# Performance work log

Hardware: AMD Instinct MI355X
Metric: run time of the kernel (lower is better)

## Reference

```python
import jax, jax.numpy as jnp
import numpy as np

N, B, T = 2048, 16, 256

def setup_inputs() -> dict:
    key = jax.random.key(0)
    k1, k2, k3, k4 = jax.random.split(key, 4)
    x = jax.random.normal(k1, (B, T, N), dtype=jnp.float32)
    weight = jax.random.normal(k2, (T, T), dtype=jnp.float32) * (1.0 / np.sqrt(T))
    bias = jax.random.normal(k3, (T,), dtype=jnp.float32) * 0.01
    # Gumbel(0,1) noise, matching torch.nn.functional.gumbel_softmax internals
    u = jax.random.uniform(k4, (N * N, 2), dtype=jnp.float32, minval=1e-6, maxval=1.0 - 1e-6)
    gumbel = -jnp.log(-jnp.log(u))
    return {"x": x, "weight": weight, "bias": bias, "gumbel": gumbel}

def reference(x, weight, bias, gumbel):
    # x: [B, T, N] -> node-major [N, B, T]
    xp = jnp.transpose(x, (2, 0, 1))
    n = xp.shape[0]
    # --- similarity-based logits (torch writes via .data -> no grad path) ---
    xs = jax.lax.stop_gradient(xp)
    x_avg = xs.mean(axis=1)                                          # [N, T]
    x_norm = x_avg / jnp.maximum(jnp.linalg.norm(x_avg, axis=-1, keepdims=True), 1e-12)
    sim = (x_norm @ x_norm.T + 1.0) * 0.5                            # [N, N] in [0,1]
    sim_flat = sim.reshape(-1)
    # gumbel_softmax(hard=True) forward: adjacency = argmax over (logits + g)
    score0 = sim_flat + gumbel[:, 0]
    score1 = (1.0 - sim_flat) + gumbel[:, 1]
    adj = (score0 > score1).astype(xp.dtype).reshape(n, n)           # directed adjacency
    # --- structural coefficient (dense, faithful to compute_structural_coeff) ---
    adj_sym = jnp.clip(adj + adj.T, 0.0, 1.0)
    nmask = jnp.clip(adj_sym + jnp.eye(n, dtype=xp.dtype), 0.0, 1.0)
    common = nmask @ nmask.T                                         # common-neighbor counts
    max_common = common.max()                                        # >= 1 (diagonal)
    valid = (adj_sym * (common > 1.0).astype(xp.dtype)) > 0
    struct = jnp.where(valid, (common / max_common) * common, 0.0)   # lambda_val = 1.0
    # edge weights only at directed-edge positions
    W = adj * struct                                                 # [src, dst]
    # --- gcn_norm (no self loops, improved=False): deg over dst, D^-1/2 W D^-1/2 ---
    deg = W.sum(axis=0)
    dinv = jnp.where(deg > 0, deg ** -0.5, 0.0)
    Wn = dinv[:, None] * W * dinv[None, :]
    # --- linear + gather-multiply-scatter aggregation (out[d] = sum_s Wn[s,d] x[s]) ---
    xw = jnp.einsum('nbt,to->nbo', xp, weight)                       # [N, B, T]
    out = jnp.einsum('sd,sbt->dbt', Wn, xw) + bias                   # [N, B, T]
    return jnp.transpose(out, (1, 2, 0))                             # [B, T, N]
```

## Files before the change

kernel.cpp:

```cpp
#include <hip/hip_runtime.h>

#define NN 2048
#define BB 16
#define TT 256

typedef unsigned short ushort_t;
typedef short bf16x8 __attribute__((ext_vector_type(8)));
typedef float f32x4 __attribute__((ext_vector_type(4)));

__device__ __forceinline__ ushort_t f2bf(float f) {
    unsigned u = __float_as_uint(f);
    return (ushort_t)((u + 0x7FFFu + ((u >> 16) & 1u)) >> 16);
}

__device__ __forceinline__ void gload16(const void* g, void* l) {
    __builtin_amdgcn_global_load_lds((const __attribute__((address_space(1))) unsigned int*)g,
                                     (__attribute__((address_space(3))) unsigned int*)l,
                                     16, 0, 0);
}

__device__ __forceinline__ void mfma_loop128(
    const ushort_t* __restrict__ Ag, size_t lda,
    const ushort_t* __restrict__ Bg, size_t ldb,
    int m0, int n0, int nkt,
    ushort_t (*As)[128][32], ushort_t (*Bs)[128][32],
    f32x4 (&acc)[4][4], int tid)
{
    const int lane = tid & 63, wave = tid >> 6;
    const int wr = wave >> 1, wc = wave & 1;
    const int r0 = tid >> 2, kc = (tid & 3) * 8;
    const int lr = lane & 15, kg = (lane >> 4) * 8;
    gload16(&Ag[(size_t)(m0 + r0) * lda + kc], &As[0][r0][kc]);
    gload16(&Bg[(size_t)(n0 + r0) * ldb + kc], &Bs[0][r0][kc]);
    gload16(&Ag[(size_t)(m0 + r0 + 64) * lda + kc], &As[0][r0 + 64][kc]);
    gload16(&Bg[(size_t)(n0 + r0 + 64) * ldb + kc], &Bs[0][r0 + 64][kc]);
    __syncthreads();
    int cur = 0;
    for (int kt = 0; kt < nkt; kt++) {
        if (kt + 1 < nkt) {
            const int k0 = (kt + 1) * 32;
            gload16(&Ag[(size_t)(m0 + r0) * lda + k0 + kc], &As[cur ^ 1][r0][kc]);
            gload16(&Bg[(size_t)(n0 + r0) * ldb + k0 + kc], &Bs[cur ^ 1][r0][kc]);
            gload16(&Ag[(size_t)(m0 + r0 + 64) * lda + k0 + kc], &As[cur ^ 1][r0 + 64][kc]);
            gload16(&Bg[(size_t)(n0 + r0 + 64) * ldb + k0 + kc], &Bs[cur ^ 1][r0 + 64][kc]);
        }
        bf16x8 af[4], bf[4];
#pragma unroll
        for (int f = 0; f < 4; f++) {
            af[f] = *(const bf16x8*)&As[cur][wr * 64 + f * 16 + lr][kg];
            bf[f] = *(const bf16x8*)&Bs[cur][wc * 64 + f * 16 + lr][kg];
        }
#pragma unroll
        for (int i = 0; i < 4; i++)
#pragma unroll
            for (int j = 0; j < 4; j++)
                acc[i][j] = __builtin_amdgcn_mfma_f32_16x16x32_bf16(af[i], bf[j], acc[i][j], 0, 0, 0);
        __syncthreads();
        cur ^= 1;
    }
}

__global__ __launch_bounds__(256) void k_colsum(const float* __restrict__ x,
                                                float* __restrict__ xsumT,
                                                float* __restrict__ ssq) {
    const int n = blockIdx.x * 256 + threadIdx.x;
    const int t = blockIdx.y;
    float s = 0.f;
#pragma unroll
    for (int b = 0; b < BB; b++) s += x[(size_t)(b * TT + t) * NN + n];
    xsumT[(size_t)t * NN + n] = s;
    atomicAdd(&ssq[n], s * s);
}

__global__ __launch_bounds__(256) void k_adj(const float* __restrict__ A,
                                             const float* __restrict__ ssq,
                                             const float* __restrict__ gumbel,
                                             ushort_t* __restrict__ adjb) {
    __shared__ __align__(16) float As[2][32][64];
    __shared__ __align__(16) float Bs[2][32][64];
    const int m0 = blockIdx.y * 64, n0 = blockIdx.x * 64;
    const int tid = threadIdx.x;
    const int tx = tid & 15, ty = tid >> 4;
    const int sr = tid >> 4, sc = (tid & 15) * 4;
    float acc[4][4];
#pragma unroll
    for (int i = 0; i < 4; i++)
#pragma unroll
        for (int j = 0; j < 4; j++) acc[i][j] = 0.f;
    gload16(&A[(size_t)sr * NN + m0 + sc], &As[0][sr][sc]);
    gload16(&A[(size_t)sr * NN + n0 + sc], &Bs[0][sr][sc]);
    gload16(&A[(size_t)(sr + 16) * NN + m0 + sc], &As[0][sr + 16][sc]);
    gload16(&A[(size_t)(sr + 16) * NN + n0 + sc], &Bs[0][sr + 16][sc]);
    __syncthreads();
    int cur = 0;
    for (int kt = 0; kt < 8; kt++) {
        if (kt + 1 < 8) {
            const int k0 = (kt + 1) * 32;
            gload16(&A[(size_t)(k0 + sr) * NN + m0 + sc], &As[cur ^ 1][sr][sc]);
            gload16(&A[(size_t)(k0 + sr) * NN + n0 + sc], &Bs[cur ^ 1][sr][sc]);
            gload16(&A[(size_t)(k0 + sr + 16) * NN + m0 + sc], &As[cur ^ 1][sr + 16][sc]);
            gload16(&A[(size_t)(k0 + sr + 16) * NN + n0 + sc], &Bs[cur ^ 1][sr + 16][sc]);
        }
#pragma unroll 16
        for (int kk = 0; kk < 32; kk++) {
            float4 a = *(const float4*)&As[cur][kk][ty * 4];
            float4 b = *(const float4*)&Bs[cur][kk][tx * 4];
            const float av[4] = {a.x, a.y, a.z, a.w};
            const float bv[4] = {b.x, b.y, b.z, b.w};
#pragma unroll
            for (int i = 0; i < 4; i++)
#pragma unroll
                for (int j = 0; j < 4; j++) acc[i][j] = fmaf(av[i], bv[j], acc[i][j]);
        }
        __syncthreads();
        cur ^= 1;
    }
    float invi[4], invj[4];
#pragma unroll
    for (int i = 0; i < 4; i++) {
        const float si = ssq[m0 + ty * 4 + i];
        invi[i] = (si > 0.f) ? rsqrtf(si) : 0.f;
        const float sj = ssq[n0 + tx * 4 + i];
        invj[i] = (sj > 0.f) ? rsqrtf(sj) : 0.f;
    }
#pragma unroll
    for (int i = 0; i < 4; i++) {
        const int gi = m0 + ty * 4 + i;
        const size_t rowb = (size_t)gi * NN + n0 + tx * 4;
#pragma unroll
        for (int j = 0; j < 4; j++) {
            const float dot = acc[i][j] * invi[i] * invj[j];
            const float2 g = *(const float2*)&gumbel[2 * (rowb + j)];
            adjb[rowb + j] = (dot > g.y - g.x) ? (ushort_t)0x3F80 : (ushort_t)0;
        }
    }
}

__global__ __launch_bounds__(256) void k_nmask(const ushort_t* __restrict__ adjb,
                                               ushort_t* __restrict__ nm) {
    __shared__ ushort_t tt[32][33];
    const int J = blockIdx.x * 32, I = blockIdx.y * 32;
    const int c = threadIdx.x & 31, r0 = threadIdx.x >> 5;
#pragma unroll
    for (int r = r0; r < 32; r += 8) tt[r][c] = adjb[(size_t)(J + r) * NN + I + c];
    __syncthreads();
#pragma unroll
    for (int r = r0; r < 32; r += 8) {
        const int gi = I + r, gj = J + c;
        const bool on = (gi == gj) || adjb[(size_t)gi * NN + gj] || tt[c][r];
        nm[(size_t)gi * NN + gj] = on ? (ushort_t)0x3F80 : (ushort_t)0;
    }
}

__global__ __launch_bounds__(256) void k_commonW(const ushort_t* __restrict__ nm,
                                                 const ushort_t* __restrict__ adjb,
                                                 float* __restrict__ W,
                                                 float* __restrict__ deg) {
    __shared__ __align__(16) ushort_t As[2][128][32];
    __shared__ __align__(16) ushort_t Bs[2][128][32];
    const int m0 = blockIdx.y * 128, n0 = blockIdx.x * 128;
    const int tid = threadIdx.x;
    const int lane = tid & 63, wave = tid >> 6;
    const int wr = wave >> 1, wc = wave & 1;
    f32x4 acc[4][4];
#pragma unroll
    for (int i = 0; i < 4; i++)
#pragma unroll
        for (int j = 0; j < 4; j++) acc[i][j] = (f32x4){0.f, 0.f, 0.f, 0.f};
    mfma_loop128(nm, NN, nm, NN, m0, n0, NN / 32, As, Bs, acc, tid);
    const int lr = lane & 15, rg = (lane >> 4) * 4;
#pragma unroll
    for (int j = 0; j < 4; j++) {
        const int gj = n0 + wc * 64 + j * 16 + lr;
        float psum = 0.f;
#pragma unroll
        for (int i = 0; i < 4; i++)
#pragma unroll
            for (int r = 0; r < 4; r++) {
                const int gi = m0 + wr * 64 + i * 16 + rg + r;
                const float cv = acc[i][j][r];
                const size_t fl = (size_t)gi * NN + gj;
                const float wv = (cv > 1.0f && adjb[fl]) ? cv * cv : 0.f;
                W[fl] = wv;
                psum += wv;
            }
        atomicAdd(&deg[gj], psum);
    }
}

__global__ __launch_bounds__(256) void k_wtn(const float* __restrict__ W,
                                             const float* __restrict__ deg,
                                             ushort_t* __restrict__ Wtn) {
    __shared__ float tt[64][65];
    const int S0 = blockIdx.x * 64, D0 = blockIdx.y * 64;
    const int c = threadIdx.x & 63, r0 = threadIdx.x >> 6;
#pragma unroll
    for (int r = r0; r < 64; r += 4) tt[r][c] = W[(size_t)(S0 + r) * NN + D0 + c];
    __syncthreads();
    const float dgs = deg[S0 + c];
    const float ds = (dgs > 0.f) ? rsqrtf(dgs) : 0.f;
#pragma unroll
    for (int r = r0; r < 64; r += 4) {
        const int d = D0 + r;
        const float dgd = deg[d];
        const float dd = (dgd > 0.f) ? rsqrtf(dgd) : 0.f;
        Wtn[(size_t)d * NN + S0 + c] = f2bf(tt[c][r] * ds * dd);
    }
}

__global__ __launch_bounds__(256) void k_xt(const float* __restrict__ x,
                                            ushort_t* __restrict__ xT) {
    __shared__ float tile[64][65];
    const int b = blockIdx.z, t0 = blockIdx.y * 64, n0 = blockIdx.x * 64;
    const int c = threadIdx.x & 63, r0 = threadIdx.x >> 6;
#pragma unroll
    for (int r = r0; r < 64; r += 4)
        tile[r][c] = x[(size_t)(b * TT + t0 + r) * NN + n0 + c];
    __syncthreads();
#pragma unroll
    for (int r = r0; r < 64; r += 4)
        xT[(size_t)(b * NN + n0 + r) * TT + t0 + c] = f2bf(tile[c][r]);
}

__global__ __launch_bounds__(256) void k_wt(const float* __restrict__ w,
                                            ushort_t* __restrict__ wT) {
    __shared__ float tile[64][65];
    const int t0 = blockIdx.y * 64, o0 = blockIdx.x * 64;
    const int c = threadIdx.x & 63, r0 = threadIdx.x >> 6;
#pragma unroll
    for (int r = r0; r < 64; r += 4)
        tile[r][c] = w[(size_t)(t0 + r) * TT + o0 + c];
    __syncthreads();
#pragma unroll
    for (int r = r0; r < 64; r += 4)
        wT[(size_t)(o0 + r) * TT + t0 + c] = f2bf(tile[c][r]);
}

__global__ __launch_bounds__(256) void k_xw(const ushort_t* __restrict__ wT,
                                            const ushort_t* __restrict__ xT,
                                            ushort_t* __restrict__ xwT) {
    __shared__ __align__(16) ushort_t As[2][128][32];
    __shared__ __align__(16) ushort_t Bs[2][128][32];
    const int b = blockIdx.z;
    const ushort_t* __restrict__ Bg = xT + (size_t)b * NN * TT;
    const int m0 = blockIdx.y * 128, n0 = blockIdx.x * 128;
    const int tid = threadIdx.x;
    const int lane = tid & 63, wave = tid >> 6;
    const int wr = wave >> 1, wc = wave & 1;
    f32x4 acc[4][4];
#pragma unroll
    for (int i = 0; i < 4; i++)
#pragma unroll
        for (int j = 0; j < 4; j++) acc[i][j] = (f32x4){0.f, 0.f, 0.f, 0.f};
    mfma_loop128(wT, TT, Bg, TT, m0, n0, TT / 32, As, Bs, acc, tid);
    const int lr = lane & 15, rg = (lane >> 4) * 4;
#pragma unroll
    for (int i = 0; i < 4; i++)
#pragma unroll
        for (int j = 0; j < 4; j++)
#pragma unroll
            for (int r = 0; r < 4; r++) {
                const int o = m0 + wr * 64 + i * 16 + rg + r;
                const int n = n0 + wc * 64 + j * 16 + lr;
                xwT[((size_t)b * TT + o) * NN + n] = f2bf(acc[i][j][r]);
            }
}

__global__ __launch_bounds__(256) void k_out(const ushort_t* __restrict__ xwT,
                                             const ushort_t* __restrict__ Wtn,
                                             const float* __restrict__ bias,
                                             float* __restrict__ out) {
    __shared__ __align__(16) ushort_t As[2][128][32];
    __shared__ __align__(16) ushort_t Bs[2][128][32];
    const int m0 = blockIdx.y * 128, n0 = blockIdx.x * 128;
    const int tid = threadIdx.x;
    const int lane = tid & 63, wave = tid >> 6;
    const int wr = wave >> 1, wc = wave & 1;
    f32x4 acc[4][4];
#pragma unroll
    for (int i = 0; i < 4; i++)
#pragma unroll
        for (int j = 0; j < 4; j++) acc[i][j] = (f32x4){0.f, 0.f, 0.f, 0.f};
    mfma_loop128(xwT, NN, Wtn, NN, m0, n0, NN / 32, As, Bs, acc, tid);
    const int lr = lane & 15, rg = (lane >> 4) * 4;
#pragma unroll
    for (int i = 0; i < 4; i++)
#pragma unroll
        for (int j = 0; j < 4; j++)
#pragma unroll
            for (int r = 0; r < 4; r++) {
                const int gm = m0 + wr * 64 + i * 16 + rg + r;
                const int gd = n0 + wc * 64 + j * 16 + lr;
                out[(size_t)gm * NN + gd] = acc[i][j][r] + bias[gm & (TT - 1)];
            }
}

extern "C" void kernel_launch(void* const* d_in, const int* in_sizes, int n_in,
                              void* d_out, int out_size, void* d_ws, size_t ws_size,
                              hipStream_t stream) {
    const float* x      = (const float*)d_in[0];
    const float* w      = (const float*)d_in[1];
    const float* bias   = (const float*)d_in[2];
    const float* gumbel = (const float*)d_in[3];
    float* out = (float*)d_out;

    char* ws = (char*)d_ws;
    float*    xsumT = (float*)(ws + 0);
    float*    ssq   = (float*)(ws + 2097152);
    float*    deg   = (float*)(ws + 2105344);
    ushort_t* adjb  = (ushort_t*)(ws + 2113536);
    ushort_t* nm    = (ushort_t*)(ws + 10502144);
    ushort_t* xT    = (ushort_t*)(ws + 2113536);
    float*    W     = (float*)(ws + 18890752);
    ushort_t* xwT   = (ushort_t*)(ws + 18890752);
    ushort_t* Wtn   = (ushort_t*)(ws + 35667968);
    ushort_t* wT    = (ushort_t*)(ws + 44056576);

    hipMemsetAsync(ws + 2097152, 0, 16384, stream);

    k_colsum <<<dim3(NN / 256, TT), 256, 0, stream>>>(x, xsumT, ssq);
    k_adj    <<<dim3(32, 32),       256, 0, stream>>>(xsumT, ssq, gumbel, adjb);
    k_nmask  <<<dim3(64, 64),       256, 0, stream>>>(adjb, nm);
    k_commonW<<<dim3(16, 16),       256, 0, stream>>>(nm, adjb, W, deg);
    k_wtn    <<<dim3(32, 32),       256, 0, stream>>>(W, deg, Wtn);
    k_xt     <<<dim3(32, 4, BB),    256, 0, stream>>>(x, xT);
    k_wt     <<<dim3(4, 4),         256, 0, stream>>>(w, wT);
    k_xw     <<<dim3(16, 2, BB),    256, 0, stream>>>(wT, xT, xwT);
    k_out    <<<dim3(16, 32),       256, 0, stream>>>(xwT, Wtn, bias, out);
}
```

Measured before the change: 310.9 us.

## Use int8 MFMA for common-neighbor GEMM, fuse colsum with transpose, shrink GEMM tiles

Stores the adjacency and neighbor masks as uint8 instead of bf16 and computes the common-neighbor counts with an int8 MFMA using integer accumulation. This halves the mask bytes and doubles the K depth per instruction. The column-sum and bf16 transpose of x are fused into one kernel so x is read once. All three GEMMs switch from 128x128 to 128x64 tiles, doubling the block count for better CU occupancy at the cost of more operand reloads.

```diff
diff --git a/kernel.cpp b/kernel.cpp
--- a/kernel.cpp
+++ b/kernel.cpp
@@ -5,8 +5,10 @@
 #define TT 256
 
 typedef unsigned short ushort_t;
+typedef unsigned char u8;
 typedef short bf16x8 __attribute__((ext_vector_type(8)));
 typedef float f32x4 __attribute__((ext_vector_type(4)));
+typedef int i32x4 __attribute__((ext_vector_type(4)));
 
 __device__ __forceinline__ ushort_t f2bf(float f) {
     unsigned u = __float_as_uint(f);
@@ -19,63 +21,118 @@
                                      16, 0, 0);
 }
 
-__device__ __forceinline__ void mfma_loop128(
+__device__ __forceinline__ void loop_bf16_128x64(
     const ushort_t* __restrict__ Ag, size_t lda,
     const ushort_t* __restrict__ Bg, size_t ldb,
     int m0, int n0, int nkt,
-    ushort_t (*As)[128][32], ushort_t (*Bs)[128][32],
-    f32x4 (&acc)[4][4], int tid)
+    ushort_t (*As)[128][32], ushort_t (*Bs)[64][32],
+    f32x4 (&acc)[4][2], int tid)
 {
     const int lane = tid & 63, wave = tid >> 6;
     const int wr = wave >> 1, wc = wave & 1;
     const int r0 = tid >> 2, kc = (tid & 3) * 8;
     const int lr = lane & 15, kg = (lane >> 4) * 8;
     gload16(&Ag[(size_t)(m0 + r0) * lda + kc], &As[0][r0][kc]);
+    gload16(&Ag[(size_t)(m0 + r0 + 64) * lda + kc], &As[0][r0 + 64][kc]);
     gload16(&Bg[(size_t)(n0 + r0) * ldb + kc], &Bs[0][r0][kc]);
-    gload16(&Ag[(size_t)(m0 + r0 + 64) * lda + kc], &As[0][r0 + 64][kc]);
-    gload16(&Bg[(size_t)(n0 + r0 + 64) * ldb + kc], &Bs[0][r0 + 64][kc]);
     __syncthreads();
     int cur = 0;
     for (int kt = 0; kt < nkt; kt++) {
         if (kt + 1 < nkt) {
             const int k0 = (kt + 1) * 32;
             gload16(&Ag[(size_t)(m0 + r0) * lda + k0 + kc], &As[cur ^ 1][r0][kc]);
+            gload16(&Ag[(size_t)(m0 + r0 + 64) * lda + k0 + kc], &As[cur ^ 1][r0 + 64][kc]);
             gload16(&Bg[(size_t)(n0 + r0) * ldb + k0 + kc], &Bs[cur ^ 1][r0][kc]);
+        }
+        bf16x8 af[4], bfj[2];
+#pragma unroll
+        for (int f = 0; f < 4; f++) af[f] = *(const bf16x8*)&As[cur][wr * 64 + f * 16 + lr][kg];
+#pragma unroll
+        for (int j = 0; j < 2; j++) bfj[j] = *(const bf16x8*)&Bs[cur][wc * 32 + j * 16 + lr][kg];
+#pragma unroll
+        for (int i = 0; i < 4; i++)
+#pragma unroll
+            for (int j = 0; j < 2; j++)
+                acc[i][j] = __builtin_amdgcn_mfma_f32_16x16x32_bf16(af[i], bfj[j], acc[i][j], 0, 0, 0);
+        __syncthreads();
+        cur ^= 1;
+    }
+}
+
+__device__ __forceinline__ void loop_i8_128x64(
+    const u8* __restrict__ Ag, size_t lda,
+    const u8* __restrict__ Bg, size_t ldb,
+    int m0, int n0, int nkt,
+    u8 (*As)[128][64], u8 (*Bs)[64][64],
+    i32x4 (&acc)[4][2], int tid)
+{
+    const int lane = tid & 63, wave = tid >> 6;
+    const int wr = wave >> 1, wc = wave & 1;
+    const int r0 = tid >> 2, kc = (tid & 3) * 16;
+    const int lr = lane & 15, kg = (lane >> 4) * 16;
+    gload16(&Ag[(size_t)(m0 + r0) * lda + kc], &As[0][r0][kc]);
+    gload16(&Ag[(size_t)(m0 + r0 + 64) * lda + kc], &As[0][r0 + 64][kc]);
+    gload16(&Bg[(size_t)(n0 + r0) * ldb + kc], &Bs[0][r0][kc]);
+    __syncthreads();
+    int cur = 0;
+    for (int kt = 0; kt < nkt; kt++) {
+        if (kt + 1 < nkt) {
+            const int k0 = (kt + 1) * 64;
+            gload16(&Ag[(size_t)(m0 + r0) * lda + k0 + kc], &As[cur ^ 1][r0][kc]);
             gload16(&Ag[(size_t)(m0 + r0 + 64) * lda + k0 + kc], &As[cur ^ 1][r0 + 64][kc]);
-            gload16(&Bg[(size_t)(n0 + r0 + 64) * ldb + k0 + kc], &Bs[cur ^ 1][r0 + 64][kc]);
-        }
-        bf16x8 af[4], bf[4];
-#pragma unroll
-        for (int f = 0; f < 4; f++) {
-            af[f] = *(const bf16x8*)&As[cur][wr * 64 + f * 16 + lr][kg];
-            bf[f] = *(const bf16x8*)&Bs[cur][wc * 64 + f * 16 + lr][kg];
-        }
+            gload16(&Bg[(size_t)(n0 + r0) * ldb + k0 + kc], &Bs[cur ^ 1][r0][kc]);
+        }
+        i32x4 af[4], bfj[2];
+#pragma unroll
+        for (int f = 0; f < 4; f++) af[f] = *(const i32x4*)&As[cur][wr * 64 + f * 16 + lr][kg];
+#pragma unroll
+        for (int j = 0; j < 2; j++) bfj[j] = *(const i32x4*)&Bs[cur][wc * 32 + j * 16 + lr][kg];
 #pragma unroll
         for (int i = 0; i < 4; i++)
 #pragma unroll
-            for (int j = 0; j < 4; j++)
-                acc[i][j] = __builtin_amdgcn_mfma_f32_16x16x32_bf16(af[i], bf[j], acc[i][j], 0, 0, 0);
+            for (int j = 0; j < 2; j++)
+                acc[i][j] = __builtin_amdgcn_mfma_i32_16x16x64_i8(af[i], bfj[j], acc[i][j], 0, 0, 0);
         __syncthreads();
         cur ^= 1;
     }
 }
 
-__global__ __launch_bounds__(256) void k_colsum(const float* __restrict__ x,
-                                                float* __restrict__ xsumT,
-                                                float* __restrict__ ssq) {
-    const int n = blockIdx.x * 256 + threadIdx.x;
-    const int t = blockIdx.y;
-    float s = 0.f;
-#pragma unroll
-    for (int b = 0; b < BB; b++) s += x[(size_t)(b * TT + t) * NN + n];
-    xsumT[(size_t)t * NN + n] = s;
-    atomicAdd(&ssq[n], s * s);
+__global__ __launch_bounds__(256) void k_xts(const float* __restrict__ x,
+                                             ushort_t* __restrict__ xT,
+                                             float* __restrict__ xsumT,
+                                             float* __restrict__ ssq) {
+    __shared__ float tile[32][33];
+    __shared__ float ssqp[32];
+    const int n0 = blockIdx.x * 32, t0 = blockIdx.y * 32;
+    const int tid = threadIdx.x;
+    const int r = tid >> 3, c4 = (tid & 7) * 4;
+    if (tid < 32) ssqp[tid] = 0.f;
+    float4 acc = {0.f, 0.f, 0.f, 0.f};
+    for (int b = 0; b < BB; b++) {
+        const float4 v = *(const float4*)&x[(size_t)((b * TT) + t0 + r) * NN + n0 + c4];
+        acc.x += v.x; acc.y += v.y; acc.z += v.z; acc.w += v.w;
+        __syncthreads();
+        tile[r][c4 + 0] = v.x; tile[r][c4 + 1] = v.y;
+        tile[r][c4 + 2] = v.z; tile[r][c4 + 3] = v.w;
+        __syncthreads();
+        ushort4 o;
+        o.x = f2bf(tile[c4 + 0][r]); o.y = f2bf(tile[c4 + 1][r]);
+        o.z = f2bf(tile[c4 + 2][r]); o.w = f2bf(tile[c4 + 3][r]);
+        *(ushort4*)&xT[(size_t)(b * NN + n0 + r) * TT + t0 + c4] = o;
+    }
+    *(float4*)&xsumT[(size_t)(t0 + r) * NN + n0 + c4] = acc;
+    atomicAdd(&ssqp[c4 + 0], acc.x * acc.x);
+    atomicAdd(&ssqp[c4 + 1], acc.y * acc.y);
+    atomicAdd(&ssqp[c4 + 2], acc.z * acc.z);
+    atomicAdd(&ssqp[c4 + 3], acc.w * acc.w);
+    __syncthreads();
+    if (tid < 32) atomicAdd(&ssq[n0 + tid], ssqp[tid]);
 }
 
 __global__ __launch_bounds__(256) void k_adj(const float* __restrict__ A,
                                              const float* __restrict__ ssq,
                                              const float* __restrict__ gumbel,
-                                             ushort_t* __restrict__ adjb) {
+                                             u8* __restrict__ adjb) {
     __shared__ __align__(16) float As[2][32][64];
     __shared__ __align__(16) float Bs[2][32][64];
     const int m0 = blockIdx.y * 64, n0 = blockIdx.x * 64;
@@ -131,14 +188,14 @@
         for (int j = 0; j < 4; j++) {
             const float dot = acc[i][j] * invi[i] * invj[j];
             const float2 g = *(const float2*)&gumbel[2 * (rowb + j)];
-            adjb[rowb + j] = (dot > g.y - g.x) ? (ushort_t)0x3F80 : (ushort_t)0;
-        }
-    }
-}
-
-__global__ __launch_bounds__(256) void k_nmask(const ushort_t* __restrict__ adjb,
-                                               ushort_t* __restrict__ nm) {
-    __shared__ ushort_t tt[32][33];
+            adjb[rowb + j] = (dot > g.y - g.x) ? (u8)1 : (u8)0;
+        }
+    }
+}
+
+__global__ __launch_bounds__(256) void k_nmask(const u8* __restrict__ adjb,
+                                               u8* __restrict__ nm) {
+    __shared__ u8 tt[32][33];
     const int J = blockIdx.x * 32, I = blockIdx.y * 32;
     const int c = threadIdx.x & 31, r0 = threadIdx.x >> 5;
 #pragma unroll
@@ -148,39 +205,40 @@
     for (int r = r0; r < 32; r += 8) {
         const int gi = I + r, gj = J + c;
         const bool on = (gi == gj) || adjb[(size_t)gi * NN + gj] || tt[c][r];
-        nm[(size_t)gi * NN + gj] = on ? (ushort_t)0x3F80 : (ushort_t)0;
-    }
-}
-
-__global__ __launch_bounds__(256) void k_commonW(const ushort_t* __restrict__ nm,
-                                                 const ushort_t* __restrict__ adjb,
+        nm[(size_t)gi * NN + gj] = on ? (u8)1 : (u8)0;
+    }
+}
+
+__global__ __launch_bounds__(256) void k_commonW(const u8* __restrict__ nm,
+                                                 const u8* __restrict__ adjb,
                                                  float* __restrict__ W,
                                                  float* __restrict__ deg) {
-    __shared__ __align__(16) ushort_t As[2][128][32];
-    __shared__ __align__(16) ushort_t Bs[2][128][32];
-    const int m0 = blockIdx.y * 128, n0 = blockIdx.x * 128;
-    const int tid = threadIdx.x;
-    const int lane = tid & 63, wave = tid >> 6;
-    const int wr = wave >> 1, wc = wave & 1;
-    f32x4 acc[4][4];
-#pragma unroll
-    for (int i = 0; i < 4; i++)
-#pragma unroll
-        for (int j = 0; j < 4; j++) acc[i][j] = (f32x4){0.f, 0.f, 0.f, 0.f};
-    mfma_loop128(nm, NN, nm, NN, m0, n0, NN / 32, As, Bs, acc, tid);
+    __shared__ __align__(16) u8 As[2][128][64];
+    __shared__ __align__(16) u8 Bs[2][64][64];
+    const int m0 = blockIdx.y * 128, n0 = blockIdx.x * 64;
+    const int tid = threadIdx.x;
+    const int lane = tid & 63, wave = tid >> 6;
+    const int wr = wave >> 1, wc = wave & 1;
+    i32x4 acc[4][2];
+#pragma unroll
+    for (int i = 0; i < 4; i++)
+#pragma unroll
+        for (int j = 0; j < 2; j++) acc[i][j] = (i32x4){0, 0, 0, 0};
+    loop_i8_128x64(nm, NN, nm, NN, m0, n0, NN / 64, As, Bs, acc, tid);
     const int lr = lane & 15, rg = (lane >> 4) * 4;
 #pragma unroll
-    for (int j = 0; j < 4; j++) {
-        const int gj = n0 + wc * 64 + j * 16 + lr;
+    for (int j = 0; j < 2; j++) {
+        const int gj = n0 + wc * 32 + j * 16 + lr;
         float psum = 0.f;
 #pragma unroll
         for (int i = 0; i < 4; i++)
 #pragma unroll
             for (int r = 0; r < 4; r++) {
                 const int gi = m0 + wr * 64 + i * 16 + rg + r;
-                const float cv = acc[i][j][r];
+                const int cv = acc[i][j][r];
                 const size_t fl = (size_t)gi * NN + gj;
-                const float wv = (cv > 1.0f && adjb[fl]) ? cv * cv : 0.f;
+                const float cf = (float)cv;
+                const float wv = (cv > 1 && adjb[fl]) ? cf * cf : 0.f;
                 W[fl] = wv;
                 psum += wv;
             }
@@ -208,20 +266,6 @@
     }
 }
 
-__global__ __launch_bounds__(256) void k_xt(const float* __restrict__ x,
-                                            ushort_t* __restrict__ xT) {
-    __shared__ float tile[64][65];
-    const int b = blockIdx.z, t0 = blockIdx.y * 64, n0 = blockIdx.x * 64;
-    const int c = threadIdx.x & 63, r0 = threadIdx.x >> 6;
-#pragma unroll
-    for (int r = r0; r < 64; r += 4)
-        tile[r][c] = x[(size_t)(b * TT + t0 + r) * NN + n0 + c];
-    __syncthreads();
-#pragma unroll
-    for (int r = r0; r < 64; r += 4)
-        xT[(size_t)(b * NN + n0 + r) * TT + t0 + c] = f2bf(tile[c][r]);
-}
-
 __global__ __launch_bounds__(256) void k_wt(const float* __restrict__ w,
                                             ushort_t* __restrict__ wT) {
     __shared__ float tile[64][65];
@@ -240,28 +284,28 @@
                                             const ushort_t* __restrict__ xT,
                                             ushort_t* __restrict__ xwT) {
     __shared__ __align__(16) ushort_t As[2][128][32];
-    __shared__ __align__(16) ushort_t Bs[2][128][32];
+    __shared__ __align__(16) ushort_t Bs[2][64][32];
     const int b = blockIdx.z;
     const ushort_t* __restrict__ Bg = xT + (size_t)b * NN * TT;
-    const int m0 = blockIdx.y * 128, n0 = blockIdx.x * 128;
-    const int tid = threadIdx.x;
-    const int lane = tid & 63, wave = tid >> 6;
-    const int wr = wave >> 1, wc = wave & 1;
-    f32x4 acc[4][4];
-#pragma unroll
-    for (int i = 0; i < 4; i++)
-#pragma unroll
-        for (int j = 0; j < 4; j++) acc[i][j] = (f32x4){0.f, 0.f, 0.f, 0.f};
-    mfma_loop128(wT, TT, Bg, TT, m0, n0, TT / 32, As, Bs, acc, tid);
+    const int m0 = blockIdx.y * 128, n0 = blockIdx.x * 64;
+    const int tid = threadIdx.x;
+    const int lane = tid & 63, wave = tid >> 6;
+    const int wr = wave >> 1, wc = wave & 1;
+    f32x4 acc[4][2];
+#pragma unroll
+    for (int i = 0; i < 4; i++)
+#pragma unroll
+        for (int j = 0; j < 2; j++) acc[i][j] = (f32x4){0.f, 0.f, 0.f, 0.f};
+    loop_bf16_128x64(wT, TT, Bg, TT, m0, n0, TT / 32, As, Bs, acc, tid);
     const int lr = lane & 15, rg = (lane >> 4) * 4;
 #pragma unroll
     for (int i = 0; i < 4; i++)
 #pragma unroll
-        for (int j = 0; j < 4; j++)
+        for (int j = 0; j < 2; j++)
 #pragma unroll
             for (int r = 0; r < 4; r++) {
                 const int o = m0 + wr * 64 + i * 16 + rg + r;
-                const int n = n0 + wc * 64 + j * 16 + lr;
+                const int n = n0 + wc * 32 + j * 16 + lr;
                 xwT[((size_t)b * TT + o) * NN + n] = f2bf(acc[i][j][r]);
             }
 }
@@ -271,26 +315,26 @@
                                              const float* __restrict__ bias,
                                              float* __restrict__ out) {
     __shared__ __align__(16) ushort_t As[2][128][32];
-    __shared__ __align__(16) ushort_t Bs[2][128][32];
-    const int m0 = blockIdx.y * 128, n0 = blockIdx.x * 128;
-    const int tid = threadIdx.x;
-    const int lane = tid & 63, wave = tid >> 6;
-    const int wr = wave >> 1, wc = wave & 1;
-    f32x4 acc[4][4];
-#pragma unroll
-    for (int i = 0; i < 4; i++)
-#pragma unroll
-        for (int j = 0; j < 4; j++) acc[i][j] = (f32x4){0.f, 0.f, 0.f, 0.f};
-    mfma_loop128(xwT, NN, Wtn, NN, m0, n0, NN / 32, As, Bs, acc, tid);
+    __shared__ __align__(16) ushort_t Bs[2][64][32];
+    const int m0 = blockIdx.y * 128, n0 = blockIdx.x * 64;
+    const int tid = threadIdx.x;
+    const int lane = tid & 63, wave = tid >> 6;
+    const int wr = wave >> 1, wc = wave & 1;
+    f32x4 acc[4][2];
+#pragma unroll
+    for (int i = 0; i < 4; i++)
+#pragma unroll
+        for (int j = 0; j < 2; j++) acc[i][j] = (f32x4){0.f, 0.f, 0.f, 0.f};
+    loop_bf16_128x64(xwT, NN, Wtn, NN, m0, n0, NN / 32, As, Bs, acc, tid);
     const int lr = lane & 15, rg = (lane >> 4) * 4;
 #pragma unroll
     for (int i = 0; i < 4; i++)
 #pragma unroll
-        for (int j = 0; j < 4; j++)
+        for (int j = 0; j < 2; j++)
 #pragma unroll
             for (int r = 0; r < 4; r++) {
                 const int gm = m0 + wr * 64 + i * 16 + rg + r;
-                const int gd = n0 + wc * 64 + j * 16 + lr;
+                const int gd = n0 + wc * 32 + j * 16 + lr;
                 out[(size_t)gm * NN + gd] = acc[i][j][r] + bias[gm & (TT - 1)];
             }
 }
@@ -308,23 +352,22 @@
     float*    xsumT = (float*)(ws + 0);
     float*    ssq   = (float*)(ws + 2097152);
     float*    deg   = (float*)(ws + 2105344);
-    ushort_t* adjb  = (ushort_t*)(ws + 2113536);
-    ushort_t* nm    = (ushort_t*)(ws + 10502144);
-    ushort_t* xT    = (ushort_t*)(ws + 2113536);
-    float*    W     = (float*)(ws + 18890752);
-    ushort_t* xwT   = (ushort_t*)(ws + 18890752);
-    ushort_t* Wtn   = (ushort_t*)(ws + 35667968);
-    ushort_t* wT    = (ushort_t*)(ws + 44056576);
+    u8*       adjb  = (u8*)(ws + 2113536);
+    u8*       nm    = (u8*)(ws + 6307840);
+    float*    W     = (float*)(ws + 10502144);
+    ushort_t* xwT   = (ushort_t*)(ws + 10502144);
+    ushort_t* Wtn   = (ushort_t*)(ws + 27279360);
+    ushort_t* xT    = (ushort_t*)(ws + 35667968);
+    ushort_t* wT    = (ushort_t*)(ws + 52445184);
 
     hipMemsetAsync(ws + 2097152, 0, 16384, stream);
 
-    k_colsum <<<dim3(NN / 256, TT), 256, 0, stream>>>(x, xsumT, ssq);
-    k_adj    <<<dim3(32, 32),       256, 0, stream>>>(xsumT, ssq, gumbel, adjb);
-    k_nmask  <<<dim3(64, 64),       256, 0, stream>>>(adjb, nm);
-    k_commonW<<<dim3(16, 16),       256, 0, stream>>>(nm, adjb, W, deg);
-    k_wtn    <<<dim3(32, 32),       256, 0, stream>>>(W, deg, Wtn);
-    k_xt     <<<dim3(32, 4, BB),    256, 0, stream>>>(x, xT);
-    k_wt     <<<dim3(4, 4),         256, 0, stream>>>(w, wT);
-    k_xw     <<<dim3(16, 2, BB),    256, 0, stream>>>(wT, xT, xwT);
-    k_out    <<<dim3(16, 32),       256, 0, stream>>>(xwT, Wtn, bias, out);
-}
+    k_xts    <<<dim3(NN / 32, TT / 32), 256, 0, stream>>>(x, xT, xsumT, ssq);
+    k_adj    <<<dim3(32, 32),           256, 0, stream>>>(xsumT, ssq, gumbel, adjb);
+    k_nmask  <<<dim3(64, 64),           256, 0, stream>>>(adjb, nm);
+    k_commonW<<<dim3(NN / 64, NN / 128),256, 0, stream>>>(nm, adjb, W, deg);
+    k_wtn    <<<dim3(32, 32),           256, 0, stream>>>(W, deg, Wtn);
+    k_wt     <<<dim3(4, 4),             256, 0, stream>>>(w, wT);
+    k_xw     <<<dim3(NN / 64, TT / 128, BB), 256, 0, stream>>>(wT, xT, xwT);
+    k_out    <<<dim3(NN / 64, (BB * TT) / 128), 256, 0, stream>>>(xwT, Wtn, bias, out);
+}
```

Result: faster. 281.3 us (-9.5%).
